# Kernel tuning notes

Hardware: AMD Instinct MI355X
Metric: run time of the kernel (lower is better)

Reference implementation:

```python
import jax, jax.numpy as jnp
import numpy as np

DIM_IN, DIM_OUT, DIM_HID = 1024, 1024, 1024
BATCH = 16384


def setup_inputs() -> dict:
    key = jax.random.key(0)
    k1, k2, k3, k4 = jax.random.split(key, 4)
    x = jax.random.normal(k1, (BATCH, DIM_IN), dtype=jnp.float32)
    # W_slow: Linear(dim_in -> dim_out + 2*dim_hidden + 1)
    W_slow_w = jax.random.normal(k2, (DIM_OUT + 2 * DIM_HID + 1, DIM_IN), dtype=jnp.float32) * (1.0 / np.sqrt(DIM_IN))
    W_slow_b = jax.random.normal(k3, (DIM_OUT + 2 * DIM_HID + 1,), dtype=jnp.float32) * 0.01
    # W_fast: Linear(dim_hidden -> dim_out), weight initialized to zero per module
    W_fast_w = jnp.zeros((DIM_OUT, DIM_HID), dtype=jnp.float32)
    W_fast_b = jax.random.normal(k4, (DIM_OUT,), dtype=jnp.float32) * 0.01
    return {"x": x, "W_slow_w": W_slow_w, "W_slow_b": W_slow_b,
            "W_fast_w": W_fast_w, "W_fast_b": W_fast_b}


def reference(x, W_slow_w, W_slow_b, W_fast_w, W_fast_b):
    B = x.shape[0]
    s = x @ W_slow_w.T + W_slow_b                      # [B, O + 2H + 1]
    k = s[:, :DIM_HID]                                 # [B, H]
    v = s[:, DIM_HID:DIM_HID + DIM_OUT]                # [B, O]
    q = s[:, DIM_HID + DIM_OUT:DIM_HID + DIM_OUT + DIM_HID]  # [B, H]
    lr = jax.nn.sigmoid(s[:, -1:])                     # [B, 1]
    # fast-weight read with softmax key
    v_bar = jax.nn.softmax(k, axis=1) @ W_fast_w.T + W_fast_b  # [B, O]
    # delta-rule outer-product update (batched, normalized by B)
    delta = jnp.einsum('bo,bh->oh', lr * (v - v_bar), jax.nn.sigmoid(k)) / B  # [O, H]
    W_new = W_fast_w + delta
    # read with updated fast weights
    return jax.nn.softmax(q, axis=1) @ W_new.T + W_fast_b  # [B, O]
```

## Files before the change

kernel.cpp:

```cpp
#include <hip/hip_runtime.h>
#include <math.h>

static constexpr int BATCH = 16384;

typedef __attribute__((ext_vector_type(8))) __bf16 bf16x8;
typedef __attribute__((ext_vector_type(4))) float f32x4;

__device__ __forceinline__ float sigm(float x) { return 1.0f / (1.0f + expf(-x)); }

__device__ __forceinline__ unsigned short f2bf(float f) {
  unsigned u = __float_as_uint(f);
  return (unsigned short)((u + 0x7fffu + ((u >> 16) & 1u)) >> 16);
}
__device__ __forceinline__ float bf2f(unsigned short u) {
  return __uint_as_float((unsigned)u << 16);
}

template <int EPI>
__global__ __launch_bounds__(512, 2) void mgemm8(
    const unsigned short* __restrict__ Ag, const unsigned short* __restrict__ Bg,
    int lda, int ldb, const float* __restrict__ bias,
    unsigned short* __restrict__ t0, unsigned short* __restrict__ t1,
    unsigned short* __restrict__ t2, float* __restrict__ Cf,
    const unsigned short* __restrict__ vTin, const float* __restrict__ lrp,
    unsigned short* __restrict__ outT, int ldT) {
  constexpr int NT = 32;
  __shared__ unsigned short As[4 * 8192];
  __shared__ unsigned short Bs[4 * 8192];
  const int tid = threadIdx.x, lane = tid & 63, w = tid >> 6;
  const int lm = lane & 15, kg = lane >> 4;
  const int wm = w >> 2, wn = w & 3;
  const int bm = blockIdx.y * 256, bn = blockIdx.x * 256;
  f32x4 acc[8][4] = {};

  int offA[8], offB[4];
#pragma unroll
  for (int i = 0; i < 8; i++) {
    int r = wm * 128 + i * 16 + lm;
    offA[i] = r * 32 + (((kg + r + (r >> 2)) & 3) << 3);
  }
#pragma unroll
  for (int j = 0; j < 4; j++) {
    int r = wn * 64 + j * 16 + lm;
    offB[j] = r * 32 + (((kg + r + (r >> 2)) & 3) << 3);
  }
  const unsigned short* gA[2];
  const unsigned short* gB[2];
  int ldsoff[2];
#pragma unroll
  for (int i = 0; i < 2; i++) {
    int r = i * 128 + w * 16 + (lane >> 2);
    int q = ((lane & 3) - r - (r >> 2)) & 3;
    gA[i] = Ag + (size_t)(bm + r) * lda + q * 8;
    gB[i] = Bg + (size_t)(bn + r) * ldb + q * 8;
    ldsoff[i] = i * 4096 + w * 512;
  }
  auto stageA = [&](int tt, int buf) {
#pragma unroll
    for (int i = 0; i < 2; i++)
      __builtin_amdgcn_global_load_lds(
          (__attribute__((address_space(1))) void*)(unsigned short*)(gA[i] + tt * 32),
          (__attribute__((address_space(3))) void*)(As + buf * 8192 + ldsoff[i]),
          16, 0, 0);
  };
  auto stageB = [&](int tt, int buf) {
#pragma unroll
    for (int i = 0; i < 2; i++)
      __builtin_amdgcn_global_load_lds(
          (__attribute__((address_space(1))) void*)(unsigned short*)(gB[i] + tt * 32),
          (__attribute__((address_space(3))) void*)(Bs + buf * 8192 + ldsoff[i]),
          16, 0, 0);
  };

  stageA(0, 0); stageB(0, 0);
  stageA(1, 1); stageB(1, 1);
  asm volatile("s_waitcnt vmcnt(4)" ::: "memory");
  __builtin_amdgcn_s_barrier();
  __builtin_amdgcn_sched_barrier(0);

  for (int t = 0; t < NT; ++t) {
    const unsigned short* Ab = As + (t & 3) * 8192;
    const unsigned short* Bb = Bs + (t & 3) * 8192;
    bf16x8 aF[4], bF[4];
#pragma unroll
    for (int i = 0; i < 4; i++) aF[i] = *(const bf16x8*)(Ab + offA[i]);
#pragma unroll
    for (int j = 0; j < 4; j++) bF[j] = *(const bf16x8*)(Bb + offB[j]);
    if (t + 2 < NT) stageA(t + 2, (t + 2) & 3);
    __builtin_amdgcn_s_barrier();
    asm volatile("s_waitcnt lgkmcnt(0)" ::: "memory");
    __builtin_amdgcn_sched_barrier(0);
    __builtin_amdgcn_s_setprio(1);
#pragma unroll
    for (int i = 0; i < 4; i++)
#pragma unroll
      for (int j = 0; j < 4; j++)
        acc[i][j] = __builtin_amdgcn_mfma_f32_16x16x32_bf16(aF[i], bF[j], acc[i][j], 0, 0, 0);
    __builtin_amdgcn_s_setprio(0);
    __builtin_amdgcn_sched_barrier(0);
    __builtin_amdgcn_s_barrier();
    bf16x8 aG[4];
#pragma unroll
    for (int i = 0; i < 4; i++) aG[i] = *(const bf16x8*)(Ab + offA[4 + i]);
    if (t + 2 < NT) stageB(t + 2, (t + 2) & 3);
    __builtin_amdgcn_s_barrier();
    asm volatile("s_waitcnt lgkmcnt(0)" ::: "memory");
    __builtin_amdgcn_sched_barrier(0);
    __builtin_amdgcn_s_setprio(1);
#pragma unroll
    for (int i = 0; i < 4; i++)
#pragma unroll
      for (int j = 0; j < 4; j++)
        acc[4 + i][j] = __builtin_amdgcn_mfma_f32_16x16x32_bf16(aG[i], bF[j], acc[4 + i][j], 0, 0, 0);
    __builtin_amdgcn_s_setprio(0);
    __builtin_amdgcn_sched_barrier(0);
    if (t < NT - 2) { asm volatile("s_waitcnt vmcnt(4)" ::: "memory"); }
    else            { asm volatile("s_waitcnt vmcnt(0)" ::: "memory"); }
    __builtin_amdgcn_s_barrier();
    __builtin_amdgcn_sched_barrier(0);
  }

#pragma unroll
  for (int i = 0; i < 8; i++) {
#pragma unroll
    for (int j = 0; j < 4; j++) {
      const int gcol = bn + wn * 64 + j * 16 + lm;
      const int grow0 = bm + wm * 128 + i * 16 + kg * 4;
      if (EPI == 0) {
        const int which = gcol >> 10;
        unsigned short* dst = which == 0 ? t0 : (which == 1 ? t1 : t2);
        const float bv = bias[gcol];
        ushort4 pk;
        pk.x = f2bf(acc[i][j][0] + bv);
        pk.y = f2bf(acc[i][j][1] + bv);
        pk.z = f2bf(acc[i][j][2] + bv);
        pk.w = f2bf(acc[i][j][3] + bv);
        *(ushort4*)(dst + (size_t)(gcol & 1023) * ldT + grow0) = pk;
      } else if (EPI == 1) {
        const float bv = bias[gcol];
        const float4 l4 = *(const float4*)(lrp + grow0);
        const ushort4 v4 = *(const ushort4*)(vTin + (size_t)gcol * ldT + grow0);
        ushort4 o;
        o.x = f2bf(l4.x * (bf2f(v4.x) - (acc[i][j][0] + bv)));
        o.y = f2bf(l4.y * (bf2f(v4.y) - (acc[i][j][1] + bv)));
        o.z = f2bf(l4.z * (bf2f(v4.z) - (acc[i][j][2] + bv)));
        o.w = f2bf(l4.w * (bf2f(v4.w) - (acc[i][j][3] + bv)));
        *(ushort4*)(outT + (size_t)gcol * ldT + grow0) = o;
      } else {
        const float bv = bias[gcol];
#pragma unroll
        for (int r = 0; r < 4; r++)
          Cf[(size_t)(grow0 + r) * 1024 + gcol] = acc[i][j][r] + bv;
      }
    }
  }
}

template <int EPI>
__global__ __launch_bounds__(256) void mgemm(
    const unsigned short* __restrict__ Ag, const unsigned short* __restrict__ Bg,
    int lda, int ldb, int ksl, const float* __restrict__ bias,
    unsigned short* __restrict__ t0, unsigned short* __restrict__ t1,
    unsigned short* __restrict__ t2, float* __restrict__ Cf,
    const unsigned short* __restrict__ vTin, const float* __restrict__ lrp,
    unsigned short* __restrict__ outT, int ldT) {
  __shared__ unsigned short As[128 * 32];
  __shared__ unsigned short Bs[128 * 32];
  const int tid = threadIdx.x, lane = tid & 63, w = tid >> 6;
  const int lm = lane & 15, kg = lane >> 4;
  const int mh = (w >> 1) * 64, nh = (w & 1) * 64;
  const int bm = blockIdx.y * 128, bn = blockIdx.x * 128;
  const int kstart = blockIdx.z * ksl, kend = kstart + ksl;
  f32x4 acc[4][4] = {};

  int offA[4], offB[4];
#pragma unroll
  for (int i = 0; i < 4; i++) {
    int rA = mh + i * 16 + lm;
    offA[i] = rA * 32 + (((kg + rA + (rA >> 2)) & 3) << 3);
    int rB = nh + i * 16 + lm;
    offB[i] = rB * 32 + (((kg + rB + (rB >> 2)) & 3) << 3);
  }
  int rowS[2], kcS[2];
#pragma unroll
  for (int t = 0; t < 2; t++) {
    int c = (w * 2 + t) * 64 + lane;
    rowS[t] = c >> 2;
    kcS[t] = ((((c & 3) - rowS[t] - (rowS[t] >> 2)) & 3) << 3);
  }

  for (int k0 = kstart; k0 < kend; k0 += 32) {
#pragma unroll
    for (int t = 0; t < 2; t++) {
      __builtin_amdgcn_global_load_lds(
          (__attribute__((address_space(1))) void*)(unsigned short*)(
              Ag + (size_t)(bm + rowS[t]) * lda + k0 + kcS[t]),
          (__attribute__((address_space(3))) void*)(As + (w * 2 + t) * 512), 16, 0, 0);
      __builtin_amdgcn_global_load_lds(
          (__attribute__((address_space(1))) void*)(unsigned short*)(
              Bg + (size_t)(bn + rowS[t]) * ldb + k0 + kcS[t]),
          (__attribute__((address_space(3))) void*)(Bs + (w * 2 + t) * 512), 16, 0, 0);
    }
    __syncthreads();
    bf16x8 aF[4], bF[4];
#pragma unroll
    for (int i = 0; i < 4; i++) {
      aF[i] = *(const bf16x8*)(As + offA[i]);
      bF[i] = *(const bf16x8*)(Bs + offB[i]);
    }
#pragma unroll
    for (int i = 0; i < 4; i++)
#pragma unroll
      for (int j = 0; j < 4; j++)
        acc[i][j] = __builtin_amdgcn_mfma_f32_16x16x32_bf16(aF[i], bF[j], acc[i][j], 0, 0, 0);
    __syncthreads();
  }

#pragma unroll
  for (int i = 0; i < 4; i++) {
#pragma unroll
    for (int j = 0; j < 4; j++) {
      const int gcol = bn + nh + j * 16 + lm;
      const int grow0 = bm + mh + i * 16 + kg * 4;
      if (EPI == 3) {
        float* dst = Cf + (size_t)blockIdx.z * (1024ull * 1024ull);
#pragma unroll
        for (int r = 0; r < 4; r++)
          dst[(size_t)(grow0 + r) * 1024 + gcol] = acc[i][j][r];
      }
    }
  }
}

template <bool DOSIG>
__global__ __launch_bounds__(256) void tsoftmax(
    const unsigned short* __restrict__ in, int ldin,
    unsigned short* __restrict__ rowout,
    unsigned short* __restrict__ sigT, int ldT) {
  __shared__ unsigned short tile[1024 * 16];
  __shared__ float red[16 * 17];
  const int t = threadIdx.x, bl = t & 15, fg = t >> 4;
  const int B0 = blockIdx.x * 16;
  const int f0 = fg * 64;
  float ls = 0.f;
  for (int f = f0; f < f0 + 64; f++) {
    unsigned short u = in[(size_t)f * ldin + B0 + bl];
    tile[f * 16 + bl] = u;
    ls += expf(bf2f(u));
  }
  red[bl * 17 + fg] = ls;
  __syncthreads();
  float tot = 0.f;
#pragma unroll
  for (int g = 0; g < 16; g++) tot += red[bl * 17 + g];
  const float inv = 1.0f / tot;
  for (int fb = f0; fb < f0 + 64; fb += 4) {
    float v[4];
#pragma unroll
    for (int e = 0; e < 4; e++) v[e] = bf2f(tile[(fb + e) * 16 + bl]);
    ushort4 o;
    o.x = f2bf(expf(v[0]) * inv);
    o.y = f2bf(expf(v[1]) * inv);
    o.z = f2bf(expf(v[2]) * inv);
    o.w = f2bf(expf(v[3]) * inv);
    *(ushort4*)(rowout + (size_t)(B0 + bl) * 1024 + fb) = o;
    if (DOSIG) {
#pragma unroll
      for (int e = 0; e < 4; e++)
        sigT[(size_t)(fb + e) * ldT + B0 + bl] = f2bf(sigm(v[e]));
    }
  }
}

__global__ __launch_bounds__(256) void lrx(const float* __restrict__ x,
                                           const float* __restrict__ Wsw,
                                           const float* __restrict__ Wsb,
                                           float* __restrict__ lrOut,
                                           unsigned short* __restrict__ xbf) {
  const int lane = threadIdx.x & 63, w = threadIdx.x >> 6;
  const int b = blockIdx.x * 4 + w;
  const float* xr = x + (size_t)b * 1024;
  const float* wr = Wsw + 3072ull * 1024ull;
  float sum = 0.f;
#pragma unroll
  for (int j = 0; j < 4; j++) {
    int f = lane + 64 * j;
    float4 xv = ((const float4*)xr)[f];
    float4 wv = ((const float4*)wr)[f];
    sum += xv.x * wv.x + xv.y * wv.y + xv.z * wv.z + xv.w * wv.w;
    ushort4 o = {f2bf(xv.x), f2bf(xv.y), f2bf(xv.z), f2bf(xv.w)};
    ((ushort4*)(xbf + (size_t)b * 1024))[f] = o;
  }
#pragma unroll
  for (int o = 32; o; o >>= 1) sum += __shfl_down(sum, o, 64);
  if (lane == 0) lrOut[b] = sigm(sum + Wsb[3072]);
}

__global__ __launch_bounds__(256) void cvt_bf(const float* __restrict__ in,
                                              unsigned short* __restrict__ outp) {
  size_t i = (size_t)blockIdx.x * 256 + threadIdx.x;
  float4 v = ((const float4*)in)[i];
  ushort4 o = {f2bf(v.x), f2bf(v.y), f2bf(v.z), f2bf(v.w)};
  ((ushort4*)outp)[i] = o;
}

__global__ __launch_bounds__(256) void wnewk(const float* __restrict__ P,
                                             const float* __restrict__ Wfw,
                                             unsigned short* __restrict__ wnbf) {
  const size_t i = (size_t)blockIdx.x * 256 + threadIdx.x;
  float s = 0.f;
#pragma unroll
  for (int z = 0; z < 8; z++) s += P[(size_t)z * (1024ull * 1024ull) + i];
  wnbf[i] = f2bf(Wfw[i] + s * (1.0f / 16384.0f));
}

extern "C" void kernel_launch(void* const* d_in, const int* in_sizes, int n_in,
                              void* d_out, int out_size, void* d_ws, size_t ws_size,
                              hipStream_t stream) {
  (void)in_sizes; (void)n_in; (void)out_size;
  const float* x   = (const float*)d_in[0];
  const float* Wsw = (const float*)d_in[1];
  const float* Wsb = (const float*)d_in[2];
  const float* Wfw = (const float*)d_in[3];
  const float* Wfb = (const float*)d_in[4];
  float* out = (float*)d_out;

  const size_t MB = 1ull << 20;
  int nc;
  if      (ws_size >= 216 * MB) nc = 1;
  else if (ws_size >= 164 * MB) nc = 2;
  else if (ws_size >= 122 * MB) nc = 4;
  else                          nc = 8;
  const size_t Bc = BATCH / nc;
  const int BcI = (int)Bc;
  const int zc = 8 / nc;
  const size_t CB = Bc * 1024 * 2;

  char* p = (char*)d_ws;
  size_t off = 0;
  auto alloc = [&](size_t bytes) {
    char* cur = p + off;
    off = (off + bytes + 255) & ~(size_t)255;
    return cur;
  };
  unsigned short* wbf  = (unsigned short*)alloc(3072ull * 1024 * 2);
  unsigned short* wfbf = (unsigned short*)alloc(1024ull * 1024 * 2);
  unsigned short* wnbf = (unsigned short*)alloc(1024ull * 1024 * 2);
  float*          lr   = (float*)alloc(BATCH * 4);
  unsigned short* qsm  = (unsigned short*)alloc((size_t)BATCH * 1024 * 2);

  unsigned short *xbf, *ksm, *kt, *Ut, *vT, *qt, *SKt;
  float* P;
  if (nc == 1) {
    char* rA = alloc(CB);
    char* rB = alloc(CB);
    char* rC = alloc(CB);
    char* rD = alloc(CB);
    char* rE = alloc(CB);
    xbf = (unsigned short*)rA; ksm = (unsigned short*)rA;
    kt  = (unsigned short*)rB; Ut  = (unsigned short*)rB;
    vT  = (unsigned short*)rC;
    qt  = (unsigned short*)rD; P   = (float*)rD;
    SKt = (unsigned short*)rE;
  } else {
    P   = (float*)alloc(32 * MB);
    char* rA = alloc(CB);
    char* rB = alloc(CB);
    xbf = (unsigned short*)rA; ksm = (unsigned short*)rA;
    kt  = (unsigned short*)rB; Ut  = (unsigned short*)rB;
    vT  = (unsigned short*)alloc(CB);
    qt  = (unsigned short*)alloc(CB);
    SKt = (unsigned short*)alloc(CB);
  }

  cvt_bf<<<dim3(3072), 256, 0, stream>>>(Wsw, wbf);
  cvt_bf<<<dim3(1024), 256, 0, stream>>>(Wfw, wfbf);

  for (int c = 0; c < nc; c++) {
    const float* xc = x + (size_t)c * Bc * 1024;
    float* lrc = lr + (size_t)c * Bc;
    lrx<<<dim3((unsigned)(Bc / 4)), 256, 0, stream>>>(xc, Wsw, Wsb, lrc, xbf);
    mgemm8<0><<<dim3(12, (unsigned)(Bc / 256)), 512, 0, stream>>>(
        xbf, wbf, 1024, 1024, Wsb, kt, vT, qt, nullptr, nullptr, nullptr,
        nullptr, BcI);
    tsoftmax<true><<<dim3((unsigned)(Bc / 16)), 256, 0, stream>>>(
        kt, BcI, ksm, SKt, BcI);
    tsoftmax<false><<<dim3((unsigned)(Bc / 16)), 256, 0, stream>>>(
        qt, BcI, qsm + (size_t)c * Bc * 1024, nullptr, BcI);
    mgemm8<1><<<dim3(4, (unsigned)(Bc / 256)), 512, 0, stream>>>(
        ksm, wfbf, 1024, 1024, Wfb, nullptr, nullptr, nullptr, nullptr,
        vT, lrc, Ut, BcI);
    mgemm<3><<<dim3(8, 8, zc), 256, 0, stream>>>(
        Ut, SKt, BcI, BcI, 2048, nullptr, nullptr, nullptr, nullptr,
        P + (size_t)c * zc * 1024 * 1024, nullptr, nullptr, nullptr, BcI);
  }

  wnewk<<<dim3(1024 * 1024 / 256), 256, 0, stream>>>(P, Wfw, wnbf);

  mgemm8<2><<<dim3(4, BATCH / 256), 512, 0, stream>>>(
      qsm, wnbf, 1024, 1024, Wfb, nullptr, nullptr, nullptr, out,
      nullptr, nullptr, nullptr, 0);
}
```

Baseline: 511.6 us.

## Collapse GEMM main loop into single phase with one barrier per tile

```diff
diff --git a/kernel.cpp b/kernel.cpp
--- a/kernel.cpp
+++ b/kernel.cpp
@@ -75,49 +75,27 @@
   stageA(0, 0); stageB(0, 0);
   stageA(1, 1); stageB(1, 1);
   asm volatile("s_waitcnt vmcnt(4)" ::: "memory");
-  __builtin_amdgcn_s_barrier();
-  __builtin_amdgcn_sched_barrier(0);
+  asm volatile("s_barrier" ::: "memory");
 
   for (int t = 0; t < NT; ++t) {
     const unsigned short* Ab = As + (t & 3) * 8192;
     const unsigned short* Bb = Bs + (t & 3) * 8192;
-    bf16x8 aF[4], bF[4];
-#pragma unroll
-    for (int i = 0; i < 4; i++) aF[i] = *(const bf16x8*)(Ab + offA[i]);
+    if (t + 2 < NT) { stageA(t + 2, (t + 2) & 3); stageB(t + 2, (t + 2) & 3); }
+    bf16x8 bF[4], aF[8];
 #pragma unroll
     for (int j = 0; j < 4; j++) bF[j] = *(const bf16x8*)(Bb + offB[j]);
-    if (t + 2 < NT) stageA(t + 2, (t + 2) & 3);
-    __builtin_amdgcn_s_barrier();
-    asm volatile("s_waitcnt lgkmcnt(0)" ::: "memory");
-    __builtin_amdgcn_sched_barrier(0);
+#pragma unroll
+    for (int i = 0; i < 8; i++) aF[i] = *(const bf16x8*)(Ab + offA[i]);
     __builtin_amdgcn_s_setprio(1);
 #pragma unroll
-    for (int i = 0; i < 4; i++)
+    for (int i = 0; i < 8; i++)
 #pragma unroll
       for (int j = 0; j < 4; j++)
         acc[i][j] = __builtin_amdgcn_mfma_f32_16x16x32_bf16(aF[i], bF[j], acc[i][j], 0, 0, 0);
     __builtin_amdgcn_s_setprio(0);
-    __builtin_amdgcn_sched_barrier(0);
-    __builtin_amdgcn_s_barrier();
-    bf16x8 aG[4];
-#pragma unroll
-    for (int i = 0; i < 4; i++) aG[i] = *(const bf16x8*)(Ab + offA[4 + i]);
-    if (t + 2 < NT) stageB(t + 2, (t + 2) & 3);
-    __builtin_amdgcn_s_barrier();
-    asm volatile("s_waitcnt lgkmcnt(0)" ::: "memory");
-    __builtin_amdgcn_sched_barrier(0);
-    __builtin_amdgcn_s_setprio(1);
-#pragma unroll
-    for (int i = 0; i < 4; i++)
-#pragma unroll
-      for (int j = 0; j < 4; j++)
-        acc[4 + i][j] = __builtin_amdgcn_mfma_f32_16x16x32_bf16(aG[i], bF[j], acc[4 + i][j], 0, 0, 0);
-    __builtin_amdgcn_s_setprio(0);
-    __builtin_amdgcn_sched_barrier(0);
     if (t < NT - 2) { asm volatile("s_waitcnt vmcnt(4)" ::: "memory"); }
     else            { asm volatile("s_waitcnt vmcnt(0)" ::: "memory"); }
-    __builtin_amdgcn_s_barrier();
-    __builtin_amdgcn_sched_barrier(0);
+    asm volatile("s_barrier" ::: "memory");
   }
 
 #pragma unroll
```

After: 552.8 us. 8.0% more time.

## Use 256x256 mgemm8 split-K for delta outer-product GEMM and swizzle block order

Applied to the files above, without the earlier changes.

```diff
diff --git a/kernel.cpp b/kernel.cpp
--- a/kernel.cpp
+++ b/kernel.cpp
@@ -30,7 +30,13 @@
   const int tid = threadIdx.x, lane = tid & 63, w = tid >> 6;
   const int lm = lane & 15, kg = lane >> 4;
   const int wm = w >> 2, wn = w & 3;
-  const int bm = blockIdx.y * 256, bn = blockIdx.x * 256;
+  const int gx = gridDim.x;
+  const int nb = gx * gridDim.y;
+  const int flat = blockIdx.y * gx + blockIdx.x;
+  int swz = flat;
+  if ((nb & 7) == 0) swz = (flat & 7) * (nb >> 3) + (flat >> 3);
+  const int bm = (swz / gx) * 256, bn = (swz % gx) * 256;
+  const int kz = (EPI == 3) ? (blockIdx.z << 10) : 0;
   f32x4 acc[8][4] = {};
 
   int offA[8], offB[4];
@@ -51,8 +57,8 @@
   for (int i = 0; i < 2; i++) {
     int r = i * 128 + w * 16 + (lane >> 2);
     int q = ((lane & 3) - r - (r >> 2)) & 3;
-    gA[i] = Ag + (size_t)(bm + r) * lda + q * 8;
-    gB[i] = Bg + (size_t)(bn + r) * ldb + q * 8;
+    gA[i] = Ag + (size_t)(bm + r) * lda + kz + q * 8;
+    gB[i] = Bg + (size_t)(bn + r) * ldb + kz + q * 8;
     ldsoff[i] = i * 4096 + w * 512;
   }
   auto stageA = [&](int tt, int buf) {
@@ -146,11 +152,16 @@
         o.z = f2bf(l4.z * (bf2f(v4.z) - (acc[i][j][2] + bv)));
         o.w = f2bf(l4.w * (bf2f(v4.w) - (acc[i][j][3] + bv)));
         *(ushort4*)(outT + (size_t)gcol * ldT + grow0) = o;
-      } else {
+      } else if (EPI == 2) {
         const float bv = bias[gcol];
 #pragma unroll
         for (int r = 0; r < 4; r++)
           Cf[(size_t)(grow0 + r) * 1024 + gcol] = acc[i][j][r] + bv;
+      } else {
+        float* dst = Cf + (size_t)blockIdx.z * (1024ull * 1024ull);
+#pragma unroll
+        for (int r = 0; r < 4; r++)
+          dst[(size_t)(grow0 + r) * 1024 + gcol] = acc[i][j][r];
       }
     }
   }
@@ -304,13 +315,14 @@
   ((ushort4*)outp)[i] = o;
 }
 
+template <int NZ>
 __global__ __launch_bounds__(256) void wnewk(const float* __restrict__ P,
                                              const float* __restrict__ Wfw,
                                              unsigned short* __restrict__ wnbf) {
   const size_t i = (size_t)blockIdx.x * 256 + threadIdx.x;
   float s = 0.f;
 #pragma unroll
-  for (int z = 0; z < 8; z++) s += P[(size_t)z * (1024ull * 1024ull) + i];
+  for (int z = 0; z < NZ; z++) s += P[(size_t)z * (1024ull * 1024ull) + i];
   wnbf[i] = f2bf(Wfw[i] + s * (1.0f / 16384.0f));
 }
 
@@ -360,7 +372,8 @@
     xbf = (unsigned short*)rA; ksm = (unsigned short*)rA;
     kt  = (unsigned short*)rB; Ut  = (unsigned short*)rB;
     vT  = (unsigned short*)rC;
-    qt  = (unsigned short*)rD; P   = (float*)rD;
+    qt  = (unsigned short*)rD;
+    P   = (float*)rC;
     SKt = (unsigned short*)rE;
   } else {
     P   = (float*)alloc(32 * MB);
@@ -390,12 +403,21 @@
     mgemm8<1><<<dim3(4, (unsigned)(Bc / 256)), 512, 0, stream>>>(
         ksm, wfbf, 1024, 1024, Wfb, nullptr, nullptr, nullptr, nullptr,
         vT, lrc, Ut, BcI);
-    mgemm<3><<<dim3(8, 8, zc), 256, 0, stream>>>(
-        Ut, SKt, BcI, BcI, 2048, nullptr, nullptr, nullptr, nullptr,
-        P + (size_t)c * zc * 1024 * 1024, nullptr, nullptr, nullptr, BcI);
-  }
-
-  wnewk<<<dim3(1024 * 1024 / 256), 256, 0, stream>>>(P, Wfw, wnbf);
+    if (nc == 1) {
+      mgemm8<3><<<dim3(4, 4, 16), 512, 0, stream>>>(
+          Ut, SKt, BcI, BcI, nullptr, nullptr, nullptr, nullptr,
+          P, nullptr, nullptr, nullptr, BcI);
+    } else {
+      mgemm<3><<<dim3(8, 8, zc), 256, 0, stream>>>(
+          Ut, SKt, BcI, BcI, 2048, nullptr, nullptr, nullptr, nullptr,
+          P + (size_t)c * zc * 1024 * 1024, nullptr, nullptr, nullptr, BcI);
+    }
+  }
+
+  if (nc == 1)
+    wnewk<16><<<dim3(1024 * 1024 / 256), 256, 0, stream>>>(P, Wfw, wnbf);
+  else
+    wnewk<8><<<dim3(1024 * 1024 / 256), 256, 0, stream>>>(P, Wfw, wnbf);
 
   mgemm8<2><<<dim3(4, BATCH / 256), 512, 0, stream>>>(
       qsm, wnbf, 1024, 1024, Wfb, nullptr, nullptr, nullptr, out,
```

Result: slower. 524.8 us (+2.6%).
